# Performance work log

Measured on AMD Instinct MI355X. Metric: run time of the kernel, lower is better.

The kernel has to match this reference:

```python
import jax, jax.numpy as jnp
import numpy as np

B = 4096
D = 1024
N = 100000
KS = (10000, 20000, 50000)


def _l2norm(x):
    # F.normalize(p=2, dim=1, eps=1e-12): x / max(||x||, eps)
    n = jnp.sqrt(jnp.sum(x * x, axis=1, keepdims=True))
    return x / jnp.maximum(n, 1e-12)


def setup_inputs() -> dict:
    key = jax.random.key(0)
    ks = jax.random.split(key, 16)
    inp = {}
    inp["anchor"] = jax.random.normal(ks[0], (B, D), jnp.float32)
    inp["index"] = jax.random.randint(ks[1], (B,), 0, N)
    for i, K in enumerate(KS):
        inp[f"inst2cluster{i}"] = jax.random.randint(ks[2 + i], (N,), 0, K)
        inp[f"centroids{i}"] = jax.random.normal(ks[5 + i], (K, D), jnp.float32)
        # density acts as a per-column temperature; keep it bounded away from 0
        inp[f"density{i}"] = jax.random.uniform(ks[8 + i], (K,), jnp.float32, 0.1, 1.0)
    return inp


def reference(anchor, centroids0, centroids1, centroids2,
              density0, density1, density2,
              index, inst2cluster0, inst2cluster1, inst2cluster2):
    Bn = anchor.shape[0]
    a = _l2norm(anchor)
    rows = jnp.arange(Bn)
    cols = jnp.arange(Bn - 1)
    # negatives[i, j] = sim[i, j + (j >= i)] -> row i without its diagonal entry
    neg_idx = cols[None, :] + (cols[None, :] >= rows[:, None])  # [B, B-1]

    scales = [(inst2cluster0, centroids0, density0),
              (inst2cluster1, centroids1, density1),
              (inst2cluster2, centroids2, density2)]
    n_scales = len(scales)

    loss = jnp.zeros(Bn, anchor.dtype)
    for i2c, cent, dens in scales:
        protos = _l2norm(cent)
        pos_id = i2c[index]                       # [B]
        sim = a @ protos[pos_id].T                # [B, B]
        pos = jnp.diagonal(sim)[:, None]          # [B, 1]
        neg = jnp.take_along_axis(sim, neg_idx, axis=1)  # [B, B-1]
        # torch broadcast: [B, B] / [B] divides column j by temp_proto[j]
        logits = jnp.concatenate([pos, neg], axis=1) / dens[pos_id][None, :]
        # CE with label 0, reduction='none'
        ce = jax.nn.logsumexp(logits, axis=1) - logits[:, 0]
        # faithful to the original: division by len(cluster_result) INSIDE the loop
        loss = (loss + ce) / n_scales
    return loss
```

## Files before the change

### kernel.cpp

```cpp
#include <hip/hip_runtime.h>

#define BB 4096
#define DD 1024
#define RTS (BB + 16)

typedef float f32x4 __attribute__((ext_vector_type(4)));
typedef short bf16x8 __attribute__((ext_vector_type(8)));

__device__ __forceinline__ unsigned short f2bf(float f) {
  unsigned u = __float_as_uint(f);
  unsigned r = u + 0x7fffu + ((u >> 16) & 1u);
  return (unsigned short)(r >> 16);
}

__device__ __forceinline__ void async16(const void* g, void* l) {
  __builtin_amdgcn_global_load_lds(
      (const __attribute__((address_space(1))) void*)g,
      (__attribute__((address_space(3))) void*)l,
      16, 0, 0);
}

__global__ __launch_bounds__(256) void norm_anchor(const float* __restrict__ x,
                                                   unsigned short* __restrict__ y) {
  __shared__ float sred[4];
  const int row = blockIdx.x;
  const int tid = threadIdx.x;
  const float4 v = ((const float4*)(x + (size_t)row * DD))[tid];
  float ss = v.x * v.x + v.y * v.y + v.z * v.z + v.w * v.w;
#pragma unroll
  for (int off = 32; off > 0; off >>= 1) ss += __shfl_xor(ss, off, 64);
  if ((tid & 63) == 0) sred[tid >> 6] = ss;
  __syncthreads();
  const float tot = sred[0] + sred[1] + sred[2] + sred[3];
  const float inv = 1.0f / fmaxf(sqrtf(tot), 1e-12f);
  ushort4 o;
  o.x = f2bf(v.x * inv);
  o.y = f2bf(v.y * inv);
  o.z = f2bf(v.z * inv);
  o.w = f2bf(v.w * inv);
  ((ushort4*)(y + (size_t)row * DD))[tid] = o;
}

__global__ __launch_bounds__(256) void gather_norm(
    const int* __restrict__ index,
    const int* __restrict__ i2c0, const int* __restrict__ i2c1, const int* __restrict__ i2c2,
    const float* __restrict__ c0, const float* __restrict__ c1, const float* __restrict__ c2,
    const float* __restrict__ d0, const float* __restrict__ d1, const float* __restrict__ d2,
    unsigned short* __restrict__ p16, float* __restrict__ rt,
    float* __restrict__ rowacc) {
  __shared__ float sred[4];
  const int j = blockIdx.x;
  const int s = blockIdx.y;
  const int tid = threadIdx.x;
  const int* i2c = (s == 0) ? i2c0 : (s == 1) ? i2c1 : i2c2;
  const float* cent = (s == 0) ? c0 : (s == 1) ? c1 : c2;
  const float* dens = (s == 0) ? d0 : (s == 1) ? d1 : d2;
  const int pid = i2c[index[j]];
  const float4 v = ((const float4*)(cent + (size_t)pid * DD))[tid];
  float ss = v.x * v.x + v.y * v.y + v.z * v.z + v.w * v.w;
#pragma unroll
  for (int off = 32; off > 0; off >>= 1) ss += __shfl_xor(ss, off, 64);
  if ((tid & 63) == 0) sred[tid >> 6] = ss;
  __syncthreads();
  const float tot = sred[0] + sred[1] + sred[2] + sred[3];
  const float inv = 1.0f / fmaxf(sqrtf(tot), 1e-12f);
  unsigned short* out = p16 + ((size_t)s * BB + j) * DD;
  ushort4 o;
  o.x = f2bf(v.x * inv);
  o.y = f2bf(v.y * inv);
  o.z = f2bf(v.z * inv);
  o.w = f2bf(v.w * inv);
  ((ushort4*)out)[tid] = o;
  if (tid == 0) rt[(size_t)s * RTS + j] = 1.0f / dens[pid];
  if (tid == 1) rowacc[(size_t)s * BB + j] = 0.0f;
}

__global__ __launch_bounds__(256) void gemm_ce_fused(const unsigned short* __restrict__ A,
                                                     const unsigned short* __restrict__ P,
                                                     const float* __restrict__ rt,
                                                     float* __restrict__ rowacc,
                                                     float* __restrict__ diag) {
  __shared__ __align__(16) unsigned short lA[128 * 32];
  __shared__ __align__(16) unsigned short lB[128 * 32];
  __shared__ float rowsum[2][128];
  const int tid = threadIdx.x;
  const int lane = tid & 63;
  const int wave = tid >> 6;
  const int m0 = blockIdx.y * 128;
  const int n0 = blockIdx.x * 128;
  const int s = blockIdx.z;
  const unsigned short* Bm = P + (size_t)s * BB * DD;
  const float* rt_s = rt + (size_t)s * RTS;

  f32x4 acc[4][4];
#pragma unroll
  for (int mi = 0; mi < 4; ++mi)
#pragma unroll
    for (int ni = 0; ni < 4; ++ni) acc[mi][ni] = (f32x4){0.f, 0.f, 0.f, 0.f};

  const int srow = lane >> 2;
  const int scol = (lane & 3) * 8;

  const int wm = (wave >> 1) * 64;
  const int wn = (wave & 1) * 64;
  const int fr = lane & 15;
  const int fk = (lane >> 4) * 8;

  for (int k0 = 0; k0 < DD; k0 += 32) {
#pragma unroll
    for (int c = 0; c < 2; ++c) {
      const int chunk = wave * 2 + c;
      const int r = chunk * 16 + srow;
      const unsigned short* ga = A + (size_t)(m0 + r) * DD + k0 + scol;
      const unsigned short* gb = Bm + (size_t)(n0 + r) * DD + k0 + scol;
      async16(ga, &lA[chunk * 512]);
      async16(gb, &lB[chunk * 512]);
    }
    __syncthreads();

    bf16x8 af[4], bfr[4];
#pragma unroll
    for (int mi = 0; mi < 4; ++mi)
      af[mi] = *(const bf16x8*)&lA[(wm + mi * 16 + fr) * 32 + fk];
#pragma unroll
    for (int ni = 0; ni < 4; ++ni)
      bfr[ni] = *(const bf16x8*)&lB[(wn + ni * 16 + fr) * 32 + fk];
#pragma unroll
    for (int mi = 0; mi < 4; ++mi)
#pragma unroll
      for (int ni = 0; ni < 4; ++ni)
        acc[mi][ni] = __builtin_amdgcn_mfma_f32_16x16x32_bf16(af[mi], bfr[ni], acc[mi][ni], 0, 0, 0);
    __syncthreads();
  }

  const int cm = (lane >> 4) * 4;
  const float rt0 = rt_s[0];
  float rtc[4], rtp[4];
#pragma unroll
  for (int ni = 0; ni < 4; ++ni) {
    const int col = n0 + wn + ni * 16 + fr;
    rtc[ni] = rt_s[col];
    rtp[ni] = rt_s[col + 1];
  }
#pragma unroll
  for (int mi = 0; mi < 4; ++mi) {
#pragma unroll
    for (int r = 0; r < 4; ++r) {
      const int rowi = m0 + wm + mi * 16 + cm + r;
      float esum = 0.f;
#pragma unroll
      for (int ni = 0; ni < 4; ++ni) {
        const int col = n0 + wn + ni * 16 + fr;
        const float v = acc[mi][ni][r];
        const float rr = (col == rowi) ? rt0 : ((col < rowi) ? rtp[ni] : rtc[ni]);
        const float l = v * rr;
        if (col == rowi) diag[(size_t)s * BB + rowi] = l;
        esum += __expf(l);
      }
#pragma unroll
      for (int off = 1; off < 16; off <<= 1) esum += __shfl_xor(esum, off, 64);
      if (fr == 0) rowsum[wave & 1][wm + mi * 16 + cm + r] = esum;
    }
  }
  __syncthreads();
  for (int t = tid; t < 128; t += 256)
    atomicAdd(&rowacc[(size_t)s * BB + m0 + t], rowsum[0][t] + rowsum[1][t]);
}

__global__ __launch_bounds__(256) void finish(const float* __restrict__ rowacc,
                                              const float* __restrict__ diag,
                                              float* __restrict__ out) {
  const int i = blockIdx.x * 256 + threadIdx.x;
  const float ce0 = logf(rowacc[i]) - diag[i];
  const float ce1 = logf(rowacc[BB + i]) - diag[BB + i];
  const float ce2 = logf(rowacc[2 * BB + i]) - diag[2 * BB + i];
  out[i] = ce0 * (1.0f / 27.0f) + ce1 * (1.0f / 9.0f) + ce2 * (1.0f / 3.0f);
}

extern "C" void kernel_launch(void* const* d_in, const int* in_sizes, int n_in,
                              void* d_out, int out_size, void* d_ws, size_t ws_size,
                              hipStream_t stream) {
  const float* anchor = (const float*)d_in[0];
  const int* index    = (const int*)d_in[1];
  const int* i2c0     = (const int*)d_in[2];
  const float* c0     = (const float*)d_in[3];
  const float* de0    = (const float*)d_in[4];
  const int* i2c1     = (const int*)d_in[5];
  const float* c1     = (const float*)d_in[6];
  const float* de1    = (const float*)d_in[7];
  const int* i2c2     = (const int*)d_in[8];
  const float* c2     = (const float*)d_in[9];
  const float* de2    = (const float*)d_in[10];

  char* ws = (char*)d_ws;
  const size_t A16_OFF = 0;
  const size_t P16_OFF = A16_OFF + (size_t)BB * DD * 2;
  const size_t RT_OFF  = P16_OFF + (size_t)3 * BB * DD * 2;
  const size_t ACC_OFF = RT_OFF + (size_t)3 * RTS * 4;
  const size_t DIA_OFF = ACC_OFF + (size_t)3 * BB * 4;

  unsigned short* a16 = (unsigned short*)(ws + A16_OFF);
  unsigned short* p16 = (unsigned short*)(ws + P16_OFF);
  float* rt     = (float*)(ws + RT_OFF);
  float* rowacc = (float*)(ws + ACC_OFF);
  float* diag   = (float*)(ws + DIA_OFF);
  float* out = (float*)d_out;

  norm_anchor<<<BB, 256, 0, stream>>>(anchor, a16);
  gather_norm<<<dim3(BB, 3), 256, 0, stream>>>(index, i2c0, i2c1, i2c2,
                                               c0, c1, c2, de0, de1, de2, p16, rt, rowacc);
  gemm_ce_fused<<<dim3(BB / 128, BB / 128, 3), 256, 0, stream>>>(a16, p16, rt, rowacc, diag);
  finish<<<BB / 256, 256, 0, stream>>>(rowacc, diag, out);
}
```

Baseline: 441.3 us.

## Use 32x32x16 MFMA with XOR-swizzled LDS and merge prep kernels

Replaces the 16x16x32 bf16 MFMA tiling with 32x32x16 MFMA tiles (2x2 per wave), which changes the fragment loads and the epilogue row mapping and shuffle width. LDS placement of each 16-byte K segment is XOR-swizzled by row to avoid bank conflicts when fragments are read. The anchor normalization and prototype gather/normalize kernels are merged into one launch with a 4-slice grid. Together these aim to cut LDS bank conflicts, instruction count per FLOP and launch overhead, at the cost of a more intricate epilogue index mapping.

```diff
diff --git a/kernel.cpp b/kernel.cpp
--- a/kernel.cpp
+++ b/kernel.cpp
@@ -4,7 +4,7 @@
 #define DD 1024
 #define RTS (BB + 16)
 
-typedef float f32x4 __attribute__((ext_vector_type(4)));
+typedef float f32x16 __attribute__((ext_vector_type(16)));
 typedef short bf16x8 __attribute__((ext_vector_type(8)));
 
 __device__ __forceinline__ unsigned short f2bf(float f) {
@@ -20,12 +20,35 @@
       16, 0, 0);
 }
 
-__global__ __launch_bounds__(256) void norm_anchor(const float* __restrict__ x,
-                                                   unsigned short* __restrict__ y) {
+__global__ __launch_bounds__(256) void prep(
+    const float* __restrict__ anchor,
+    const int* __restrict__ index,
+    const int* __restrict__ i2c0, const int* __restrict__ i2c1, const int* __restrict__ i2c2,
+    const float* __restrict__ c0, const float* __restrict__ c1, const float* __restrict__ c2,
+    const float* __restrict__ d0, const float* __restrict__ d1, const float* __restrict__ d2,
+    unsigned short* __restrict__ a16, unsigned short* __restrict__ p16,
+    float* __restrict__ rt, float* __restrict__ rowacc) {
   __shared__ float sred[4];
-  const int row = blockIdx.x;
+  const int j = blockIdx.x;
+  const int y = blockIdx.y;
   const int tid = threadIdx.x;
-  const float4 v = ((const float4*)(x + (size_t)row * DD))[tid];
+  const float* srcrow;
+  unsigned short* dstrow;
+  if (y == 0) {
+    srcrow = anchor + (size_t)j * DD;
+    dstrow = a16 + (size_t)j * DD;
+  } else {
+    const int s = y - 1;
+    const int* i2c = (s == 0) ? i2c0 : (s == 1) ? i2c1 : i2c2;
+    const float* cent = (s == 0) ? c0 : (s == 1) ? c1 : c2;
+    const float* dens = (s == 0) ? d0 : (s == 1) ? d1 : d2;
+    const int pid = i2c[index[j]];
+    srcrow = cent + (size_t)pid * DD;
+    dstrow = p16 + ((size_t)s * BB + j) * DD;
+    if (tid == 0) rt[(size_t)s * RTS + j] = 1.0f / dens[pid];
+    if (tid == 1) rowacc[(size_t)s * BB + j] = 0.0f;
+  }
+  const float4 v = ((const float4*)srcrow)[tid];
   float ss = v.x * v.x + v.y * v.y + v.z * v.z + v.w * v.w;
 #pragma unroll
   for (int off = 32; off > 0; off >>= 1) ss += __shfl_xor(ss, off, 64);
@@ -38,41 +61,7 @@
   o.y = f2bf(v.y * inv);
   o.z = f2bf(v.z * inv);
   o.w = f2bf(v.w * inv);
-  ((ushort4*)(y + (size_t)row * DD))[tid] = o;
-}
-
-__global__ __launch_bounds__(256) void gather_norm(
-    const int* __restrict__ index,
-    const int* __restrict__ i2c0, const int* __restrict__ i2c1, const int* __restrict__ i2c2,
-    const float* __restrict__ c0, const float* __restrict__ c1, const float* __restrict__ c2,
-    const float* __restrict__ d0, const float* __restrict__ d1, const float* __restrict__ d2,
-    unsigned short* __restrict__ p16, float* __restrict__ rt,
-    float* __restrict__ rowacc) {
-  __shared__ float sred[4];
-  const int j = blockIdx.x;
-  const int s = blockIdx.y;
-  const int tid = threadIdx.x;
-  const int* i2c = (s == 0) ? i2c0 : (s == 1) ? i2c1 : i2c2;
-  const float* cent = (s == 0) ? c0 : (s == 1) ? c1 : c2;
-  const float* dens = (s == 0) ? d0 : (s == 1) ? d1 : d2;
-  const int pid = i2c[index[j]];
-  const float4 v = ((const float4*)(cent + (size_t)pid * DD))[tid];
-  float ss = v.x * v.x + v.y * v.y + v.z * v.z + v.w * v.w;
-#pragma unroll
-  for (int off = 32; off > 0; off >>= 1) ss += __shfl_xor(ss, off, 64);
-  if ((tid & 63) == 0) sred[tid >> 6] = ss;
-  __syncthreads();
-  const float tot = sred[0] + sred[1] + sred[2] + sred[3];
-  const float inv = 1.0f / fmaxf(sqrtf(tot), 1e-12f);
-  unsigned short* out = p16 + ((size_t)s * BB + j) * DD;
-  ushort4 o;
-  o.x = f2bf(v.x * inv);
-  o.y = f2bf(v.y * inv);
-  o.z = f2bf(v.z * inv);
-  o.w = f2bf(v.w * inv);
-  ((ushort4*)out)[tid] = o;
-  if (tid == 0) rt[(size_t)s * RTS + j] = 1.0f / dens[pid];
-  if (tid == 1) rowacc[(size_t)s * BB + j] = 0.0f;
+  ((ushort4*)dstrow)[tid] = o;
 }
 
 __global__ __launch_bounds__(256) void gemm_ce_fused(const unsigned short* __restrict__ A,
@@ -92,74 +81,86 @@
   const unsigned short* Bm = P + (size_t)s * BB * DD;
   const float* rt_s = rt + (size_t)s * RTS;
 
-  f32x4 acc[4][4];
-#pragma unroll
-  for (int mi = 0; mi < 4; ++mi)
-#pragma unroll
-    for (int ni = 0; ni < 4; ++ni) acc[mi][ni] = (f32x4){0.f, 0.f, 0.f, 0.f};
+  f32x16 acc[2][2];
+#pragma unroll
+  for (int tm = 0; tm < 2; ++tm)
+#pragma unroll
+    for (int tn = 0; tn < 2; ++tn)
+#pragma unroll
+      for (int e = 0; e < 16; ++e) acc[tm][tn][e] = 0.f;
 
   const int srow = lane >> 2;
-  const int scol = (lane & 3) * 8;
+  const int kseg = (lane & 3) ^ ((lane >> 2) & 3);
 
   const int wm = (wave >> 1) * 64;
   const int wn = (wave & 1) * 64;
-  const int fr = lane & 15;
-  const int fk = (lane >> 4) * 8;
+  const int r31 = lane & 31;
+  const int h = lane >> 5;
 
   for (int k0 = 0; k0 < DD; k0 += 32) {
 #pragma unroll
-    for (int c = 0; c < 2; ++c) {
-      const int chunk = wave * 2 + c;
-      const int r = chunk * 16 + srow;
-      const unsigned short* ga = A + (size_t)(m0 + r) * DD + k0 + scol;
-      const unsigned short* gb = Bm + (size_t)(n0 + r) * DD + k0 + scol;
+    for (int cc = 0; cc < 2; ++cc) {
+      const int chunk = wave * 2 + cc;
+      const int row = chunk * 16 + srow;
+      const unsigned short* ga = A + (size_t)(m0 + row) * DD + k0 + kseg * 8;
+      const unsigned short* gb = Bm + (size_t)(n0 + row) * DD + k0 + kseg * 8;
       async16(ga, &lA[chunk * 512]);
       async16(gb, &lB[chunk * 512]);
     }
     __syncthreads();
 
-    bf16x8 af[4], bfr[4];
-#pragma unroll
-    for (int mi = 0; mi < 4; ++mi)
-      af[mi] = *(const bf16x8*)&lA[(wm + mi * 16 + fr) * 32 + fk];
-#pragma unroll
-    for (int ni = 0; ni < 4; ++ni)
-      bfr[ni] = *(const bf16x8*)&lB[(wn + ni * 16 + fr) * 32 + fk];
-#pragma unroll
-    for (int mi = 0; mi < 4; ++mi)
-#pragma unroll
-      for (int ni = 0; ni < 4; ++ni)
-        acc[mi][ni] = __builtin_amdgcn_mfma_f32_16x16x32_bf16(af[mi], bfr[ni], acc[mi][ni], 0, 0, 0);
+#pragma unroll
+    for (int ks = 0; ks < 2; ++ks) {
+      const int kl = ks * 2 + h;
+      bf16x8 af[2], bfr[2];
+#pragma unroll
+      for (int tm = 0; tm < 2; ++tm) {
+        const int row = wm + tm * 32 + r31;
+        const int kpos = kl ^ (row & 3);
+        af[tm] = *(const bf16x8*)&lA[row * 32 + kpos * 8];
+      }
+#pragma unroll
+      for (int tn = 0; tn < 2; ++tn) {
+        const int row = wn + tn * 32 + r31;
+        const int kpos = kl ^ (row & 3);
+        bfr[tn] = *(const bf16x8*)&lB[row * 32 + kpos * 8];
+      }
+#pragma unroll
+      for (int tm = 0; tm < 2; ++tm)
+#pragma unroll
+        for (int tn = 0; tn < 2; ++tn)
+          acc[tm][tn] = __builtin_amdgcn_mfma_f32_32x32x16_bf16(af[tm], bfr[tn], acc[tm][tn], 0, 0, 0);
+    }
     __syncthreads();
   }
 
-  const int cm = (lane >> 4) * 4;
   const float rt0 = rt_s[0];
-  float rtc[4], rtp[4];
-#pragma unroll
-  for (int ni = 0; ni < 4; ++ni) {
-    const int col = n0 + wn + ni * 16 + fr;
-    rtc[ni] = rt_s[col];
-    rtp[ni] = rt_s[col + 1];
-  }
-#pragma unroll
-  for (int mi = 0; mi < 4; ++mi) {
-#pragma unroll
-    for (int r = 0; r < 4; ++r) {
-      const int rowi = m0 + wm + mi * 16 + cm + r;
+  float rtc[2], rtp[2];
+#pragma unroll
+  for (int tn = 0; tn < 2; ++tn) {
+    const int col = n0 + wn + tn * 32 + r31;
+    rtc[tn] = rt_s[col];
+    rtp[tn] = rt_s[col + 1];
+  }
+#pragma unroll
+  for (int tm = 0; tm < 2; ++tm) {
+#pragma unroll
+    for (int rg = 0; rg < 16; ++rg) {
+      const int rloc = (rg & 3) + 8 * (rg >> 2) + 4 * h;
+      const int grow = m0 + wm + tm * 32 + rloc;
       float esum = 0.f;
 #pragma unroll
-      for (int ni = 0; ni < 4; ++ni) {
-        const int col = n0 + wn + ni * 16 + fr;
-        const float v = acc[mi][ni][r];
-        const float rr = (col == rowi) ? rt0 : ((col < rowi) ? rtp[ni] : rtc[ni]);
+      for (int tn = 0; tn < 2; ++tn) {
+        const int col = n0 + wn + tn * 32 + r31;
+        const float v = acc[tm][tn][rg];
+        const float rr = (col == grow) ? rt0 : ((col < grow) ? rtp[tn] : rtc[tn]);
         const float l = v * rr;
-        if (col == rowi) diag[(size_t)s * BB + rowi] = l;
+        if (col == grow) diag[(size_t)s * BB + grow] = l;
         esum += __expf(l);
       }
 #pragma unroll
-      for (int off = 1; off < 16; off <<= 1) esum += __shfl_xor(esum, off, 64);
-      if (fr == 0) rowsum[wave & 1][wm + mi * 16 + cm + r] = esum;
+      for (int off = 1; off < 32; off <<= 1) esum += __shfl_xor(esum, off, 64);
+      if (r31 == 0) rowsum[wave & 1][wm + tm * 32 + rloc] = esum;
     }
   }
   __syncthreads();
@@ -206,9 +207,9 @@
   float* diag   = (float*)(ws + DIA_OFF);
   float* out = (float*)d_out;
 
-  norm_anchor<<<BB, 256, 0, stream>>>(anchor, a16);
-  gather_norm<<<dim3(BB, 3), 256, 0, stream>>>(index, i2c0, i2c1, i2c2,
-                                               c0, c1, c2, de0, de1, de2, p16, rt, rowacc);
+  prep<<<dim3(BB, 4), 256, 0, stream>>>(anchor, index, i2c0, i2c1, i2c2,
+                                        c0, c1, c2, de0, de1, de2,
+                                        a16, p16, rt, rowacc);
   gemm_ce_fused<<<dim3(BB / 128, BB / 128, 3), 256, 0, stream>>>(a16, p16, rt, rowacc, diag);
   finish<<<BB / 256, 256, 0, stream>>>(rowacc, diag, out);
 }
```

Result: slower. 472.1 us (+7.0%).
